# Optimization experiments

Measured on AMD Instinct MI355X. Metric: run time of the kernel, lower is better.

The kernel has to match this reference:

```python
import jax, jax.numpy as jnp
import numpy as np

N = 100000   # nodes
E = 1600000  # edges
F = 64       # input node features
H = 64       # hidden dim
G = 512      # graphs in batch


def setup_inputs() -> dict:
    key = jax.random.key(0)
    ks = jax.random.split(key, 10)
    x = jax.random.normal(ks[0], (N, F), dtype=jnp.float32)
    edge_index = jax.random.randint(ks[1], (2, E), 0, N, dtype=jnp.int32)
    batch = jnp.sort(jax.random.randint(ks[2], (N,), 0, G, dtype=jnp.int32))
    s = 1.0 / np.sqrt(H)
    W1 = jax.random.normal(ks[3], (F, H), dtype=jnp.float32) * s
    b1 = jnp.zeros((H,), jnp.float32)
    W2 = jax.random.normal(ks[4], (H, H), dtype=jnp.float32) * s
    b2 = jnp.zeros((H,), jnp.float32)
    W3 = jax.random.normal(ks[5], (H, H), dtype=jnp.float32) * s
    b3 = jnp.zeros((H,), jnp.float32)
    return {"x": x, "edge_index": edge_index, "batch": batch,
            "W1": W1, "b1": b1, "W2": W2, "b2": b2, "W3": W3, "b3": b3}


def _gcn_conv(x, W, b, src, dst, dinv):
    # PyG GCNConv: h = x @ W; aggregate with sym-normalized adjacency incl. self-loops; + bias
    h = x @ W                                  # [N, H]
    norm = dinv[src] * dinv[dst]               # [E]
    agg = jax.ops.segment_sum(h[src] * norm[:, None], dst, num_segments=N)
    agg = agg + h * (dinv * dinv)[:, None]     # self-loop contribution
    return agg + b


def reference(x, edge_index, batch, W1, b1, W2, b2, W3, b3):
    src, dst = edge_index[0], edge_index[1]
    # degree with self-loops (counted on dst, as in PyG)
    deg = jax.ops.segment_sum(jnp.ones((E,), x.dtype), dst, num_segments=N) + 1.0
    dinv = jax.lax.rsqrt(deg)
    h = jax.nn.relu(_gcn_conv(x, W1, b1, src, dst, dinv))
    h = jax.nn.relu(_gcn_conv(h, W2, b2, src, dst, dinv))
    h = _gcn_conv(h, W3, b3, src, dst, dinv)
    # global mean pool over graphs
    sums = jax.ops.segment_sum(h, batch, num_segments=G)          # [G, H]
    cnts = jax.ops.segment_sum(jnp.ones((N,), h.dtype), batch, num_segments=G)
    return sums / jnp.maximum(cnts, 1.0)[:, None]
```

## Files before the change

### kernel.cpp

```cpp
#include <hip/hip_runtime.h>

#define N_NODES 100000
#define N_EDGES 1600000
#define FDIM 64
#define NGRAPH 512
#define NB 782
#define NWG 256
#define CHUNK 6250
#define DWG 64
#define DCHUNK ((N_NODES + DWG - 1) / DWG)
#define MAXD 128

__device__ __forceinline__ unsigned short f2bf(float v) {
    unsigned int x = __float_as_uint(v);
    x += 0x7FFF + ((x >> 16) & 1);
    return (unsigned short)(x >> 16);
}

__global__ void scan_block(const int* __restrict__ in, int* __restrict__ excl,
                           int* __restrict__ blocksums, int n) {
    __shared__ int lds[256];
    int t = threadIdx.x;
    int base = blockIdx.x * 1024 + t * 4;
    int v0 = (base     < n) ? in[base]     : 0;
    int v1 = (base + 1 < n) ? in[base + 1] : 0;
    int v2 = (base + 2 < n) ? in[base + 2] : 0;
    int v3 = (base + 3 < n) ? in[base + 3] : 0;
    int s = v0 + v1 + v2 + v3;
    lds[t] = s;
    __syncthreads();
    for (int off = 1; off < 256; off <<= 1) {
        int x = (t >= off) ? lds[t - off] : 0;
        __syncthreads();
        lds[t] += x;
        __syncthreads();
    }
    int thrExcl = lds[t] - s;
    if (t == 255) blocksums[blockIdx.x] = lds[255];
    if (base     < n) excl[base]     = thrExcl;
    if (base + 1 < n) excl[base + 1] = thrExcl + v0;
    if (base + 2 < n) excl[base + 2] = thrExcl + v0 + v1;
    if (base + 3 < n) excl[base + 3] = thrExcl + v0 + v1 + v2;
}

__global__ void scan_top(int* __restrict__ blocksums, int nb, int* __restrict__ out, int n) {
    if (threadIdx.x == 0 && blockIdx.x == 0) {
        int run = 0;
        for (int i = 0; i < nb; ++i) { int v = blocksums[i]; blocksums[i] = run; run += v; }
        out[n] = run;
    }
}

__global__ void scan_add(int* __restrict__ out, const int* __restrict__ blocksums, int n) {
    int i = blockIdx.x * blockDim.x + threadIdx.x;
    if (i < n) out[i] += blocksums[i >> 10];
}

__global__ __launch_bounds__(256) void hist_kernel(const int* __restrict__ dst,
                                                   int* __restrict__ hist, int E) {
    __shared__ int h[NB];
    int t = threadIdx.x, wg = blockIdx.x;
    for (int i = t; i < NB; i += 256) h[i] = 0;
    __syncthreads();
    int beg = wg * CHUNK, end = min(beg + CHUNK, E);
    for (int i = beg + t; i < end; i += 256) atomicAdd(&h[dst[i] >> 7], 1);
    __syncthreads();
    for (int i = t; i < NB; i += 256) hist[i * NWG + wg] = h[i];
}

__global__ __launch_bounds__(256) void bin_kernel(const int* __restrict__ src,
                                                  const int* __restrict__ dst,
                                                  const int* __restrict__ scannedH,
                                                  int* __restrict__ ebin, int E) {
    __shared__ int base[NB];
    __shared__ int cur[NB];
    int t = threadIdx.x, wg = blockIdx.x;
    for (int i = t; i < NB; i += 256) { base[i] = scannedH[i * NWG + wg]; cur[i] = 0; }
    __syncthreads();
    int beg = wg * CHUNK, end = min(beg + CHUNK, E);
    for (int i = beg + t; i < end; i += 256) {
        int d = dst[i];
        int b = d >> 7;
        int p = base[b] + atomicAdd(&cur[b], 1);
        ebin[p] = ((d & 127) << 17) | src[i];
    }
}

__global__ __launch_bounds__(256) void csr_sort2(const int* __restrict__ ebin,
                                                 const int* __restrict__ scannedH,
                                                 int* __restrict__ csr_src,
                                                 int* __restrict__ offsets,
                                                 float* __restrict__ dinv, int E) {
    __shared__ int cnt[128];
    __shared__ int seg[128];
    __shared__ int cur[128];
    __shared__ int buf[4352];
    int t = threadIdx.x, b = blockIdx.x;
    int nbase = b << 7;
    int nodes = min(128, N_NODES - nbase);
    int bstart = scannedH[b * NWG];
    int bend = (b == NB - 1) ? E : scannedH[(b + 1) * NWG];
    if (t < 128) cnt[t] = 0;
    __syncthreads();
    for (int i = bstart + t; i < bend; i += 256) atomicAdd(&cnt[ebin[i] >> 17], 1);
    __syncthreads();
    if (t < 128) seg[t] = cnt[t];
    __syncthreads();
    for (int off = 1; off < 128; off <<= 1) {
        int v = 0;
        if (t < 128 && t >= off) v = seg[t - off];
        __syncthreads();
        if (t < 128) seg[t] += v;
        __syncthreads();
    }
    if (t < nodes) {
        int excl = seg[t] - cnt[t];
        offsets[nbase + t] = bstart + excl;
        dinv[nbase + t] = rsqrtf((float)cnt[t] + 1.0f);
        cur[t] = excl;
    }
    if (b == 0 && t == 0) offsets[N_NODES] = E;
    __syncthreads();
    for (int i = bstart + t; i < bend; i += 256) {
        int v = ebin[i];
        int p = atomicAdd(&cur[v >> 17], 1);
        buf[p] = v & 0x1FFFF;
    }
    __syncthreads();
    int span = bend - bstart;
    for (int i = t; i < span; i += 256) csr_src[bstart + i] = buf[i];
}

__global__ __launch_bounds__(256) void histD_kernel(const int* __restrict__ offsets,
                                                    int* __restrict__ histD) {
    __shared__ int h[MAXD];
    int t = threadIdx.x, wg = blockIdx.x;
    if (t < MAXD) h[t] = 0;
    __syncthreads();
    int beg = wg * DCHUNK, end = min(beg + DCHUNK, N_NODES);
    for (int i = beg + t; i < end; i += 256) {
        int d = min(offsets[i + 1] - offsets[i], MAXD - 1);
        atomicAdd(&h[d], 1);
    }
    __syncthreads();
    if (t < MAXD) histD[t * DWG + wg] = h[t];
}

__global__ __launch_bounds__(256) void binD_kernel(const int* __restrict__ offsets,
                                                   const int* __restrict__ scannedD,
                                                   int* __restrict__ perm) {
    __shared__ int base[MAXD];
    __shared__ int cur[MAXD];
    int t = threadIdx.x, wg = blockIdx.x;
    if (t < MAXD) { base[t] = scannedD[t * DWG + wg]; cur[t] = 0; }
    __syncthreads();
    int beg = wg * DCHUNK, end = min(beg + DCHUNK, N_NODES);
    for (int i = beg + t; i < end; i += 256) {
        int d = min(offsets[i + 1] - offsets[i], MAXD - 1);
        int pos = base[d] + atomicAdd(&cur[d], 1);
        perm[pos] = i;
    }
}

__global__ __launch_bounds__(256) void gemm64(const float* __restrict__ X,
                                              const float* __restrict__ W,
                                              const float* __restrict__ dinv,
                                              unsigned short* __restrict__ Hout, int n) {
    __shared__ float Ws[64 * 68];
    __shared__ float Xs[64 * 68];
    int t = threadIdx.x;
    int r0 = blockIdx.x * 64;

    #pragma unroll
    for (int kk = 0; kk < 16; ++kk) {
        int idx = t + kk * 256;
        int r = idx >> 6, c = idx & 63;
        Ws[r * 68 + c] = W[idx];
        float v = (r0 + r < n) ? X[(size_t)(r0 + r) * FDIM + c] : 0.0f;
        Xs[c * 68 + r] = v;
    }
    __syncthreads();

    int rg = (t >> 4) << 2;
    int cg = (t & 15) << 2;
    float4 acc0 = {0, 0, 0, 0}, acc1 = {0, 0, 0, 0};
    float4 acc2 = {0, 0, 0, 0}, acc3 = {0, 0, 0, 0};

    #pragma unroll 8
    for (int k = 0; k < 64; ++k) {
        float4 xv = *(const float4*)&Xs[k * 68 + rg];
        float4 wv = *(const float4*)&Ws[k * 68 + cg];
        acc0.x += xv.x * wv.x; acc0.y += xv.x * wv.y; acc0.z += xv.x * wv.z; acc0.w += xv.x * wv.w;
        acc1.x += xv.y * wv.x; acc1.y += xv.y * wv.y; acc1.z += xv.y * wv.z; acc1.w += xv.y * wv.w;
        acc2.x += xv.z * wv.x; acc2.y += xv.z * wv.y; acc2.z += xv.z * wv.z; acc2.w += xv.z * wv.w;
        acc3.x += xv.w * wv.x; acc3.y += xv.w * wv.y; acc3.z += xv.w * wv.z; acc3.w += xv.w * wv.w;
    }

    float4 accs[4] = {acc0, acc1, acc2, acc3};
    #pragma unroll
    for (int i = 0; i < 4; ++i) {
        int row = r0 + rg + i;
        if (row < n) {
            float sc = dinv[row];
            unsigned int u0 = (unsigned int)f2bf(accs[i].x * sc) | ((unsigned int)f2bf(accs[i].y * sc) << 16);
            unsigned int u1 = (unsigned int)f2bf(accs[i].z * sc) | ((unsigned int)f2bf(accs[i].w * sc) << 16);
            *(uint2*)&Hout[(size_t)row * FDIM + cg] = make_uint2(u0, u1);
        }
    }
}

__global__ __launch_bounds__(256) void gather_pn(const unsigned short* __restrict__ hs,
                                                 const int* __restrict__ csr_src,
                                                 const int* __restrict__ offsets,
                                                 const int* __restrict__ perm,
                                                 const float* __restrict__ dinv,
                                                 const float* __restrict__ bias,
                                                 float* __restrict__ outb,
                                                 int n, int do_relu) {
    int slot = (blockIdx.x * 256 + threadIdx.x) >> 3;
    int p = threadIdx.x & 7;
    if (slot >= n) return;
    int node = perm[slot];
    int beg = offsets[node], end = offsets[node + 1];

    float a0 = 0, a1 = 0, a2 = 0, a3 = 0, a4 = 0, a5 = 0, a6 = 0, a7 = 0;
    int k = beg;
    for (; k + 1 < end; k += 2) {
        int s0 = csr_src[k], s1 = csr_src[k + 1];
        uint4 v0 = *(const uint4*)(hs + ((size_t)s0 << 6) + (p << 3));
        uint4 v1 = *(const uint4*)(hs + ((size_t)s1 << 6) + (p << 3));
        a0 += __uint_as_float(v0.x << 16); a1 += __uint_as_float(v0.x & 0xFFFF0000u);
        a2 += __uint_as_float(v0.y << 16); a3 += __uint_as_float(v0.y & 0xFFFF0000u);
        a4 += __uint_as_float(v0.z << 16); a5 += __uint_as_float(v0.z & 0xFFFF0000u);
        a6 += __uint_as_float(v0.w << 16); a7 += __uint_as_float(v0.w & 0xFFFF0000u);
        a0 += __uint_as_float(v1.x << 16); a1 += __uint_as_float(v1.x & 0xFFFF0000u);
        a2 += __uint_as_float(v1.y << 16); a3 += __uint_as_float(v1.y & 0xFFFF0000u);
        a4 += __uint_as_float(v1.z << 16); a5 += __uint_as_float(v1.z & 0xFFFF0000u);
        a6 += __uint_as_float(v1.w << 16); a7 += __uint_as_float(v1.w & 0xFFFF0000u);
    }
    if (k < end) {
        int s0 = csr_src[k];
        uint4 v0 = *(const uint4*)(hs + ((size_t)s0 << 6) + (p << 3));
        a0 += __uint_as_float(v0.x << 16); a1 += __uint_as_float(v0.x & 0xFFFF0000u);
        a2 += __uint_as_float(v0.y << 16); a3 += __uint_as_float(v0.y & 0xFFFF0000u);
        a4 += __uint_as_float(v0.z << 16); a5 += __uint_as_float(v0.z & 0xFFFF0000u);
        a6 += __uint_as_float(v0.w << 16); a7 += __uint_as_float(v0.w & 0xFFFF0000u);
    }
    uint4 sv = *(const uint4*)(hs + ((size_t)node << 6) + (p << 3));
    float dd = dinv[node];
    int fb = p << 3;
    const float4* bp = (const float4*)(bias + fb);
    float4 bv0 = bp[0], bv1 = bp[1];
    float o0 = dd * (a0 + __uint_as_float(sv.x << 16))        + bv0.x;
    float o1 = dd * (a1 + __uint_as_float(sv.x & 0xFFFF0000u)) + bv0.y;
    float o2 = dd * (a2 + __uint_as_float(sv.y << 16))        + bv0.z;
    float o3 = dd * (a3 + __uint_as_float(sv.y & 0xFFFF0000u)) + bv0.w;
    float o4 = dd * (a4 + __uint_as_float(sv.z << 16))        + bv1.x;
    float o5 = dd * (a5 + __uint_as_float(sv.z & 0xFFFF0000u)) + bv1.y;
    float o6 = dd * (a6 + __uint_as_float(sv.w << 16))        + bv1.z;
    float o7 = dd * (a7 + __uint_as_float(sv.w & 0xFFFF0000u)) + bv1.w;
    if (do_relu) {
        o0 = fmaxf(o0, 0.0f); o1 = fmaxf(o1, 0.0f); o2 = fmaxf(o2, 0.0f); o3 = fmaxf(o3, 0.0f);
        o4 = fmaxf(o4, 0.0f); o5 = fmaxf(o5, 0.0f); o6 = fmaxf(o6, 0.0f); o7 = fmaxf(o7, 0.0f);
    }
    float4* op = (float4*)(outb + (size_t)node * FDIM + fb);
    op[0] = make_float4(o0, o1, o2, o3);
    op[1] = make_float4(o4, o5, o6, o7);
}

__global__ void gstart_kernel(const int* __restrict__ batch, int* __restrict__ gstart, int n) {
    int g = blockIdx.x * blockDim.x + threadIdx.x;
    if (g > NGRAPH) return;
    if (g == NGRAPH) { gstart[NGRAPH] = n; return; }
    int lo = 0, hi = n;
    while (lo < hi) {
        int mid = (lo + hi) >> 1;
        if (batch[mid] < g) lo = mid + 1; else hi = mid;
    }
    gstart[g] = lo;
}

__global__ __launch_bounds__(256) void pool2(const float* __restrict__ h,
                                             const int* __restrict__ gstart,
                                             float* __restrict__ out) {
    __shared__ float red[4][64];
    int g = blockIdx.x;
    int beg = gstart[g], end = gstart[g + 1];
    int w = threadIdx.x >> 6, lane = threadIdx.x & 63;
    float acc = 0.0f;
    for (int i = beg + w; i < end; i += 4)
        acc += h[(size_t)i * FDIM + lane];
    red[w][lane] = acc;
    __syncthreads();
    if (w == 0) {
        float tot = red[0][lane] + red[1][lane] + red[2][lane] + red[3][lane];
        float cnt = (float)(end - beg);
        out[(size_t)g * FDIM + lane] = tot / fmaxf(cnt, 1.0f);
    }
}

extern "C" void kernel_launch(void* const* d_in, const int* in_sizes, int n_in,
                              void* d_out, int out_size, void* d_ws, size_t ws_size,
                              hipStream_t stream) {
    const float* x     = (const float*)d_in[0];
    const int*   ei    = (const int*)d_in[1];
    const int*   batch = (const int*)d_in[2];
    const float* W1    = (const float*)d_in[3];
    const float* b1    = (const float*)d_in[4];
    const float* W2    = (const float*)d_in[5];
    const float* b2    = (const float*)d_in[6];
    const float* W3    = (const float*)d_in[7];
    const float* b3    = (const float*)d_in[8];
    float* out = (float*)d_out;

    const int N = N_NODES, E = N_EDGES;
    const int* src = ei;
    const int* dst = ei + E;

    char* ws = (char*)d_ws;
    float*          dinv    = (float*)         (ws + 0);
    int*            offsets = (int*)           (ws + 400128);
    int*            csr_src = (int*)           (ws + 800256);
    float*          bufA    = (float*)         (ws + 7200384);
    unsigned short* hbf     = (unsigned short*)(ws + 32800384);
    int*            gstart  = (int*)           (ws + 45600384);
    int*            perm    = (int*)           (ws + 45602560);
    int*            scannedD= (int*)           (ws + 46002688);
    int*            blocksumsD=(int*)          (ws + 46035584);
    int* scannedH   = (int*)(ws + 7200384);
    int* blocksumsH = (int*)(ws + 8201216);
    int* ebin       = (int*)(ws + 8202240);

    hist_kernel<<<NWG, 256, 0, stream>>>(dst, scannedH, E);
    const int nH = NB * NWG;
    const int nScanH = (nH + 1023) / 1024;
    scan_block<<<nScanH, 256, 0, stream>>>(scannedH, scannedH, blocksumsH, nH);
    scan_top<<<1, 64, 0, stream>>>(blocksumsH, nScanH, scannedH, nH);
    scan_add<<<(nH + 255) / 256, 256, 0, stream>>>(scannedH, blocksumsH, nH);
    bin_kernel<<<NWG, 256, 0, stream>>>(src, dst, scannedH, ebin, E);
    csr_sort2<<<NB, 256, 0, stream>>>(ebin, scannedH, csr_src, offsets, dinv, E);

    histD_kernel<<<DWG, 256, 0, stream>>>(offsets, scannedD);
    const int nD = MAXD * DWG;
    const int nScanD = (nD + 1023) / 1024;
    scan_block<<<nScanD, 256, 0, stream>>>(scannedD, scannedD, blocksumsD, nD);
    scan_top<<<1, 64, 0, stream>>>(blocksumsD, nScanD, scannedD, nD);
    scan_add<<<(nD + 255) / 256, 256, 0, stream>>>(scannedD, blocksumsD, nD);
    binD_kernel<<<DWG, 256, 0, stream>>>(offsets, scannedD, perm);

    gstart_kernel<<<3, 256, 0, stream>>>(batch, gstart, N);

    const int gemmGrid   = (N + 63) / 64;
    const int gatherGrid = (N * 8 + 255) / 256;

    gemm64<<<gemmGrid, 256, 0, stream>>>(x, W1, dinv, hbf, N);
    gather_pn<<<gatherGrid, 256, 0, stream>>>(hbf, csr_src, offsets, perm, dinv, b1, bufA, N, 1);

    gemm64<<<gemmGrid, 256, 0, stream>>>(bufA, W2, dinv, hbf, N);
    gather_pn<<<gatherGrid, 256, 0, stream>>>(hbf, csr_src, offsets, perm, dinv, b2, bufA, N, 1);

    gemm64<<<gemmGrid, 256, 0, stream>>>(bufA, W3, dinv, hbf, N);
    gather_pn<<<gatherGrid, 256, 0, stream>>>(hbf, csr_src, offsets, perm, dinv, b3, bufA, N, 0);

    pool2<<<NGRAPH, 256, 0, stream>>>(bufA, gstart, out);
}
```

Measured before the change: 287.1 us.

## Widen edge histogram grid, parallelize top-level scan, unroll gather by four

```diff
diff --git a/kernel.cpp b/kernel.cpp
--- a/kernel.cpp
+++ b/kernel.cpp
@@ -5,8 +5,8 @@
 #define FDIM 64
 #define NGRAPH 512
 #define NB 782
-#define NWG 256
-#define CHUNK 6250
+#define NWG 1024
+#define CHUNK 1563
 #define DWG 64
 #define DCHUNK ((N_NODES + DWG - 1) / DWG)
 #define MAXD 128
@@ -43,12 +43,29 @@
     if (base + 3 < n) excl[base + 3] = thrExcl + v0 + v1 + v2;
 }
 
-__global__ void scan_top(int* __restrict__ blocksums, int nb, int* __restrict__ out, int n) {
-    if (threadIdx.x == 0 && blockIdx.x == 0) {
-        int run = 0;
-        for (int i = 0; i < nb; ++i) { int v = blocksums[i]; blocksums[i] = run; run += v; }
-        out[n] = run;
-    }
+__global__ void scan_top2(int* __restrict__ blocksums, int nb, int* __restrict__ out, int n) {
+    __shared__ int lds[256];
+    int t = threadIdx.x;
+    int base = t * 4;
+    int v0 = (base     < nb) ? blocksums[base]     : 0;
+    int v1 = (base + 1 < nb) ? blocksums[base + 1] : 0;
+    int v2 = (base + 2 < nb) ? blocksums[base + 2] : 0;
+    int v3 = (base + 3 < nb) ? blocksums[base + 3] : 0;
+    int s = v0 + v1 + v2 + v3;
+    lds[t] = s;
+    __syncthreads();
+    for (int off = 1; off < 256; off <<= 1) {
+        int x = (t >= off) ? lds[t - off] : 0;
+        __syncthreads();
+        lds[t] += x;
+        __syncthreads();
+    }
+    int excl = lds[t] - s;
+    if (base     < nb) blocksums[base]     = excl;
+    if (base + 1 < nb) blocksums[base + 1] = excl + v0;
+    if (base + 2 < nb) blocksums[base + 2] = excl + v0 + v1;
+    if (base + 3 < nb) blocksums[base + 3] = excl + v0 + v1 + v2;
+    if (t == 255) out[n] = lds[255];
 }
 
 __global__ void scan_add(int* __restrict__ out, const int* __restrict__ blocksums, int n) {
@@ -225,10 +242,12 @@
 
     float a0 = 0, a1 = 0, a2 = 0, a3 = 0, a4 = 0, a5 = 0, a6 = 0, a7 = 0;
     int k = beg;
-    for (; k + 1 < end; k += 2) {
-        int s0 = csr_src[k], s1 = csr_src[k + 1];
+    for (; k + 3 < end; k += 4) {
+        int s0 = csr_src[k], s1 = csr_src[k + 1], s2 = csr_src[k + 2], s3 = csr_src[k + 3];
         uint4 v0 = *(const uint4*)(hs + ((size_t)s0 << 6) + (p << 3));
         uint4 v1 = *(const uint4*)(hs + ((size_t)s1 << 6) + (p << 3));
+        uint4 v2 = *(const uint4*)(hs + ((size_t)s2 << 6) + (p << 3));
+        uint4 v3 = *(const uint4*)(hs + ((size_t)s3 << 6) + (p << 3));
         a0 += __uint_as_float(v0.x << 16); a1 += __uint_as_float(v0.x & 0xFFFF0000u);
         a2 += __uint_as_float(v0.y << 16); a3 += __uint_as_float(v0.y & 0xFFFF0000u);
         a4 += __uint_as_float(v0.z << 16); a5 += __uint_as_float(v0.z & 0xFFFF0000u);
@@ -237,8 +256,16 @@
         a2 += __uint_as_float(v1.y << 16); a3 += __uint_as_float(v1.y & 0xFFFF0000u);
         a4 += __uint_as_float(v1.z << 16); a5 += __uint_as_float(v1.z & 0xFFFF0000u);
         a6 += __uint_as_float(v1.w << 16); a7 += __uint_as_float(v1.w & 0xFFFF0000u);
-    }
-    if (k < end) {
+        a0 += __uint_as_float(v2.x << 16); a1 += __uint_as_float(v2.x & 0xFFFF0000u);
+        a2 += __uint_as_float(v2.y << 16); a3 += __uint_as_float(v2.y & 0xFFFF0000u);
+        a4 += __uint_as_float(v2.z << 16); a5 += __uint_as_float(v2.z & 0xFFFF0000u);
+        a6 += __uint_as_float(v2.w << 16); a7 += __uint_as_float(v2.w & 0xFFFF0000u);
+        a0 += __uint_as_float(v3.x << 16); a1 += __uint_as_float(v3.x & 0xFFFF0000u);
+        a2 += __uint_as_float(v3.y << 16); a3 += __uint_as_float(v3.y & 0xFFFF0000u);
+        a4 += __uint_as_float(v3.z << 16); a5 += __uint_as_float(v3.z & 0xFFFF0000u);
+        a6 += __uint_as_float(v3.w << 16); a7 += __uint_as_float(v3.w & 0xFFFF0000u);
+    }
+    for (; k < end; ++k) {
         int s0 = csr_src[k];
         uint4 v0 = *(const uint4*)(hs + ((size_t)s0 << 6) + (p << 3));
         a0 += __uint_as_float(v0.x << 16); a1 += __uint_as_float(v0.x & 0xFFFF0000u);
@@ -328,14 +355,14 @@
     int*            scannedD= (int*)           (ws + 46002688);
     int*            blocksumsD=(int*)          (ws + 46035584);
     int* scannedH   = (int*)(ws + 7200384);
-    int* blocksumsH = (int*)(ws + 8201216);
-    int* ebin       = (int*)(ws + 8202240);
+    int* blocksumsH = (int*)(ws + 10403584);
+    int* ebin       = (int*)(ws + 10407936);
 
     hist_kernel<<<NWG, 256, 0, stream>>>(dst, scannedH, E);
     const int nH = NB * NWG;
     const int nScanH = (nH + 1023) / 1024;
     scan_block<<<nScanH, 256, 0, stream>>>(scannedH, scannedH, blocksumsH, nH);
-    scan_top<<<1, 64, 0, stream>>>(blocksumsH, nScanH, scannedH, nH);
+    scan_top2<<<1, 256, 0, stream>>>(blocksumsH, nScanH, scannedH, nH);
     scan_add<<<(nH + 255) / 256, 256, 0, stream>>>(scannedH, blocksumsH, nH);
     bin_kernel<<<NWG, 256, 0, stream>>>(src, dst, scannedH, ebin, E);
     csr_sort2<<<NB, 256, 0, stream>>>(ebin, scannedH, csr_src, offsets, dinv, E);
@@ -344,7 +371,7 @@
     const int nD = MAXD * DWG;
     const int nScanD = (nD + 1023) / 1024;
     scan_block<<<nScanD, 256, 0, stream>>>(scannedD, scannedD, blocksumsD, nD);
-    scan_top<<<1, 64, 0, stream>>>(blocksumsD, nScanD, scannedD, nD);
+    scan_top2<<<1, 256, 0, stream>>>(blocksumsD, nScanD, scannedD, nD);
     scan_add<<<(nD + 255) / 256, 256, 0, stream>>>(scannedD, blocksumsD, nD);
     binD_kernel<<<DWG, 256, 0, stream>>>(offsets, scannedD, perm);
 
```

After: 274.9 us. 1.04x faster.
